# Kernel tuning notes

Measured on AMD Instinct MI355X. Metric: run time of the kernel, lower is better.

Reference implementation:

```python
import jax, jax.numpy as jnp
import numpy as np

N_NODES = 100000
N_EDGES = 1200000
C = 64            # hidden_channels == in_channels
HEADS = 4
HEAD_D = C // HEADS
EDGE_D = 16
N_LAYERS = 3
NUM_GRAPHS = 128


def setup_inputs() -> dict:
    key = jax.random.key(0)
    ks = jax.random.split(key, 24)
    x = jax.random.normal(ks[0], (N_NODES, C), dtype=jnp.float32)
    edge_index = jax.random.randint(ks[1], (2, N_EDGES), 0, N_NODES, dtype=jnp.int64)
    edge_attr = jax.random.normal(ks[2], (N_EDGES, EDGE_D), dtype=jnp.float32)
    batch = jnp.sort(jax.random.randint(ks[3], (N_NODES,), 0, NUM_GRAPHS, dtype=jnp.int64))
    s = 1.0 / np.sqrt(C)
    se = 1.0 / np.sqrt(EDGE_D)
    inp = {
        "x": x, "edge_index": edge_index, "edge_attr": edge_attr, "batch": batch,
        "Wq": jax.random.normal(ks[4], (N_LAYERS, C, C), jnp.float32) * s,
        "bq": jnp.zeros((N_LAYERS, C), jnp.float32),
        "Wk": jax.random.normal(ks[5], (N_LAYERS, C, C), jnp.float32) * s,
        "bk": jnp.zeros((N_LAYERS, C), jnp.float32),
        "Wv": jax.random.normal(ks[6], (N_LAYERS, C, C), jnp.float32) * s,
        "bv": jnp.zeros((N_LAYERS, C), jnp.float32),
        "We": jax.random.normal(ks[7], (N_LAYERS, EDGE_D, C), jnp.float32) * se,
        "be": jnp.zeros((N_LAYERS, C), jnp.float32),
        "Wskip": jax.random.normal(ks[8], (N_LAYERS, C, C), jnp.float32) * s,
        "bskip": jnp.zeros((N_LAYERS, C), jnp.float32),
        "lin1_w": jax.random.normal(ks[9], (C, C), jnp.float32) * s,
        "lin1_b": jnp.zeros((C,), jnp.float32),
        "lin2_w": jax.random.normal(ks[10], (C, 1), jnp.float32) * s,
        "lin2_b": jnp.zeros((1,), jnp.float32),
    }
    return inp


def _transformer_conv(x, src, dst, edge_attr, Wq, bq, Wk, bk, Wv, bv, We, be, Ws, bs):
    """PyG-style TransformerConv: edge-softmax attention with edge features."""
    n = x.shape[0]
    e = src.shape[0]
    q = (x @ Wq + bq)[dst].reshape(e, HEADS, HEAD_D)          # query at target i
    ea = (edge_attr @ We + be).reshape(e, HEADS, HEAD_D)      # shared edge proj
    k = (x @ Wk + bk)[src].reshape(e, HEADS, HEAD_D) + ea
    v = (x @ Wv + bv)[src].reshape(e, HEADS, HEAD_D) + ea
    logit = jnp.einsum('ehd,ehd->eh', q, k) / jnp.sqrt(jnp.float32(HEAD_D))  # [E,H]
    # numerically-stable softmax over edges sharing the same destination node
    m = jax.ops.segment_max(logit, dst, num_segments=n)       # [N,H]
    ex = jnp.exp(logit - m[dst])
    denom = jax.ops.segment_sum(ex, dst, num_segments=n)      # [N,H]
    alpha = ex / jnp.maximum(denom[dst], 1e-16)
    agg = jax.ops.segment_sum(alpha[:, :, None] * v, dst, num_segments=n)   # [N,H,D]
    return agg.reshape(n, HEADS * HEAD_D) + x @ Ws + bs       # root/skip weight


def reference(x, edge_index, edge_attr, batch, Wq, bq, Wk, bk, Wv, bv, We, be,
              Wskip, bskip, lin1_w, lin1_b, lin2_w, lin2_b):
    src, dst = edge_index[0], edge_index[1]
    h = x
    for l in range(N_LAYERS):
        h = _transformer_conv(h, src, dst, edge_attr,
                              Wq[l], bq[l], Wk[l], bk[l], Wv[l], bv[l],
                              We[l], be[l], Wskip[l], bskip[l])
        if l < N_LAYERS - 1:
            h = jax.nn.relu(h)
    # global mean pool over graphs
    sums = jax.ops.segment_sum(h, batch, num_segments=NUM_GRAPHS)            # [G,C]
    cnt = jax.ops.segment_sum(jnp.ones((h.shape[0], 1), h.dtype), batch,
                              num_segments=NUM_GRAPHS)
    pooled = sums / jnp.maximum(cnt, 1.0)
    out = jax.nn.relu(pooled @ lin1_w + lin1_b)
    return (out @ lin2_w + lin2_b).squeeze(-1)                               # [G]
```

## Files before the change

### kernel.cpp

```cpp
#include <hip/hip_runtime.h>
#include <hip/hip_bf16.h>

#define NODES_C 64
#define HEADS 4
#define HEAD_D 16

__device__ __forceinline__ unsigned short f32_to_bf16(float f) {
    unsigned int x = __float_as_uint(f);
    unsigned int r = x + 0x7fffu + ((x >> 16) & 1u);
    return (unsigned short)(r >> 16);
}
#define BF16_DEC(h) __uint_as_float(((unsigned int)(h)) << 16)

__global__ void count_k(const int* __restrict__ dst, int E, int* __restrict__ deg) {
    int e = blockIdx.x * blockDim.x + threadIdx.x;
    if (e < E) atomicAdd(&deg[dst[e]], 1);
}

__global__ __launch_bounds__(1024) void scan_chunk(const int* __restrict__ deg,
                                                   int* __restrict__ excl,
                                                   int* __restrict__ chunkSums, int N) {
    __shared__ int buf[1024];
    int i = blockIdx.x * 1024 + threadIdx.x;
    int v = (i < N) ? deg[i] : 0;
    buf[threadIdx.x] = v;
    __syncthreads();
    for (int off = 1; off < 1024; off <<= 1) {
        int t = (threadIdx.x >= off) ? buf[threadIdx.x - off] : 0;
        __syncthreads();
        buf[threadIdx.x] += t;
        __syncthreads();
    }
    if (i < N) excl[i] = buf[threadIdx.x] - v;
    if (threadIdx.x == 1023) chunkSums[blockIdx.x] = buf[1023];
}

__global__ __launch_bounds__(128) void scan_sums(int* __restrict__ chunkSums, int nChunks) {
    __shared__ int buf[128];
    int v = (threadIdx.x < nChunks) ? chunkSums[threadIdx.x] : 0;
    buf[threadIdx.x] = v;
    __syncthreads();
    for (int off = 1; off < 128; off <<= 1) {
        int t = (threadIdx.x >= off) ? buf[threadIdx.x - off] : 0;
        __syncthreads();
        buf[threadIdx.x] += t;
        __syncthreads();
    }
    if (threadIdx.x < nChunks) chunkSums[threadIdx.x] = buf[threadIdx.x] - v;
}

__global__ void scan_add(int* __restrict__ excl, const int* __restrict__ chunkSums,
                         int N, int E) {
    int i = blockIdx.x * blockDim.x + threadIdx.x;
    if (i < N) excl[i] += chunkSums[i >> 10];
    if (i == 0) excl[N] = E;
}

__global__ void fill_k(const int* __restrict__ dst, int E,
                       const int* __restrict__ row_start, int* __restrict__ cursor,
                       int* __restrict__ csr) {
    int e = blockIdx.x * blockDim.x + threadIdx.x;
    if (e < E) {
        int d = dst[e];
        int pos = atomicAdd(&cursor[d], 1);
        csr[row_start[d] + pos] = e;
    }
}

__global__ void sort_rows_k(const int* __restrict__ row_start, int* __restrict__ csr,
                            int N) {
    int i = blockIdx.x * blockDim.x + threadIdx.x;
    if (i >= N) return;
    int beg = row_start[i], end = row_start[i + 1];
    for (int p = beg + 1; p < end; ++p) {
        int key = csr[p];
        int j = p - 1;
        while (j >= beg && csr[j] > key) { csr[j + 1] = csr[j]; --j; }
        csr[j + 1] = key;
    }
}

__global__ void gather_edges(const int* __restrict__ csr, const int* __restrict__ srcA,
                             const float4* __restrict__ ea4,
                             int* __restrict__ csr_src,
                             unsigned short* __restrict__ csr_eah, int E) {
    int t = blockIdx.x * blockDim.x + threadIdx.x;
    int p = t >> 2, q = t & 3;
    if (p < E) {
        int e = csr[p];
        if (q == 0) csr_src[p] = srcA[e];
        float4 v = ea4[(size_t)e * 4 + q];
        ushort4 h;
        h.x = f32_to_bf16(v.x);  h.y = f32_to_bf16(v.y);
        h.z = f32_to_bf16(v.z);  h.w = f32_to_bf16(v.w);
        *(ushort4*)(csr_eah + (size_t)p * 16 + q * 4) = h;
    }
}

#define GB 16
__global__ __launch_bounds__(128) void gemm_qkvs(
    const float* __restrict__ Hin,
    const float* __restrict__ Wq, const float* __restrict__ bq,
    const float* __restrict__ Wk, const float* __restrict__ bk,
    const float* __restrict__ Wv, const float* __restrict__ bv,
    const float* __restrict__ Ws, const float* __restrict__ bs,
    float* __restrict__ Q, unsigned short* __restrict__ KVh,
    float* __restrict__ Ssk, int N)
{
    int g = threadIdx.x >> 6;
    int c = threadIdx.x & 63;
    const float* W1 = (g == 0) ? Wq : Wv;
    const float* b1 = (g == 0) ? bq : bv;
    const float* W2 = (g == 0) ? Wk : Ws;
    const float* b2 = (g == 0) ? bk : bs;

    float w1[64], w2[64];
#pragma unroll
    for (int t = 0; t < 64; ++t) {
        w1[t] = W1[t * 64 + c];
        w2[t] = W2[t * 64 + c];
    }
    float bias1 = b1[c], bias2 = b2[c];

    __shared__ __align__(16) float hrow[GB][64];

    for (int base = blockIdx.x * GB; base < N; base += gridDim.x * GB) {
        int nn = min(GB, N - base);
        __syncthreads();
        for (int idx = threadIdx.x; idx < nn * 64; idx += 128)
            hrow[idx >> 6][idx & 63] = Hin[base * 64 + idx];
        __syncthreads();
        for (int r = 0; r < nn; ++r) {
            const float4* h4 = (const float4*)hrow[r];
            float acc1 = bias1, acc2 = bias2;
#pragma unroll
            for (int t4 = 0; t4 < 16; ++t4) {
                float4 hv = h4[t4];
                acc1 += hv.x * w1[4 * t4 + 0];
                acc1 += hv.y * w1[4 * t4 + 1];
                acc1 += hv.z * w1[4 * t4 + 2];
                acc1 += hv.w * w1[4 * t4 + 3];
                acc2 += hv.x * w2[4 * t4 + 0];
                acc2 += hv.y * w2[4 * t4 + 1];
                acc2 += hv.z * w2[4 * t4 + 2];
                acc2 += hv.w * w2[4 * t4 + 3];
            }
            size_t row = (size_t)(base + r);
            if (g == 0) {
                Q[row * 64 + c] = acc1;
                KVh[row * 128 + 2 * c] = f32_to_bf16(acc2);
            } else {
                KVh[row * 128 + 2 * c + 1] = f32_to_bf16(acc1);
                Ssk[row * 64 + c] = acc2;
            }
        }
    }
}

#define KV_DECODE(u, kf, vf)                                \
    kf = __uint_as_float((u) << 16);                        \
    vf = __uint_as_float((u) & 0xffff0000u);

__global__ __launch_bounds__(256) void attn_pre(
    const float* __restrict__ Q, const unsigned int* __restrict__ KVu,
    const float* __restrict__ Ssk,
    const int* __restrict__ row_start, const int* __restrict__ csr_src,
    const unsigned short* __restrict__ csr_eah,
    const float* __restrict__ We, const float* __restrict__ be,
    float* __restrict__ Hout, int N, int doRelu)
{
    __shared__ float weS[16 * 68];
    for (int idx = threadIdx.x; idx < 1024; idx += 256)
        weS[(idx >> 6) * 68 + (idx & 63)] = We[idx];
    __syncthreads();

    int lane = threadIdx.x & 63;
    int tl = lane & 15;
    int hb = lane & 48;
    float wcol[16];
#pragma unroll
    for (int t = 0; t < 16; ++t) wcol[t] = weS[t * 68 + lane];
    float beL = be[lane];

    int gwave  = (blockIdx.x * blockDim.x + threadIdx.x) >> 6;
    int nwaves = (gridDim.x * blockDim.x) >> 6;

    const float4* wr4 = (const float4*)(weS + tl * 68 + hb);
    float4 wa = wr4[0], wb = wr4[1], wc4 = wr4[2], wd = wr4[3];

    for (int i = gwave; i < N; i += nwaves) {
        float q = Q[(size_t)i * 64 + lane];

        const float4* qh4 = (const float4*)(Q + (size_t)i * 64 + hb);
        float4 qa = qh4[0], qb4 = qh4[1], qc4 = qh4[2], qd = qh4[3];
        float G = qa.x * wa.x + qa.y * wa.y + qa.z * wa.z + qa.w * wa.w
                + qb4.x * wb.x + qb4.y * wb.y + qb4.z * wb.z + qb4.w * wb.w
                + qc4.x * wc4.x + qc4.y * wc4.y + qc4.z * wc4.z + qc4.w * wc4.w
                + qd.x * wd.x + qd.y * wd.y + qd.z * wd.z + qd.w * wd.w;
        float rb = q * beL;
#pragma unroll
        for (int off = 8; off >= 1; off >>= 1) rb += __shfl_xor(rb, off, 16);
        float qbase = rb * 0.25f;

        int beg = row_start[i], end = row_start[i + 1];
        float m = -INFINITY, s = 0.f, acc = 0.f, z = 0.f;

        int p = beg;
        if (p + 7 < end) {
            int j0 = csr_src[p],     j1 = csr_src[p + 1];
            int j2 = csr_src[p + 2], j3 = csr_src[p + 3];
            int j4 = csr_src[p + 4], j5 = csr_src[p + 5];
            int j6 = csr_src[p + 6], j7 = csr_src[p + 7];
            const unsigned short* eh = csr_eah + (size_t)p * 16 + tl;
            float a0 = BF16_DEC(eh[0]),  a1 = BF16_DEC(eh[16]);
            float a2 = BF16_DEC(eh[32]), a3 = BF16_DEC(eh[48]);
            float a4 = BF16_DEC(eh[64]), a5 = BF16_DEC(eh[80]);
            float a6 = BF16_DEC(eh[96]), a7 = BF16_DEC(eh[112]);

            do {
                unsigned int u0 = KVu[(size_t)j0 * 64 + lane];
                unsigned int u1 = KVu[(size_t)j1 * 64 + lane];
                unsigned int u2 = KVu[(size_t)j2 * 64 + lane];
                unsigned int u3 = KVu[(size_t)j3 * 64 + lane];
                unsigned int u4 = KVu[(size_t)j4 * 64 + lane];
                unsigned int u5 = KVu[(size_t)j5 * 64 + lane];
                unsigned int u6 = KVu[(size_t)j6 * 64 + lane];
                unsigned int u7 = KVu[(size_t)j7 * 64 + lane];

                int pn = p + 8;
                bool more = (pn + 7 < end);
                int jn0 = j0, jn1 = j1, jn2 = j2, jn3 = j3;
                int jn4 = j4, jn5 = j5, jn6 = j6, jn7 = j7;
                float an0 = a0, an1 = a1, an2 = a2, an3 = a3;
                float an4 = a4, an5 = a5, an6 = a6, an7 = a7;
                if (more) {
                    jn0 = csr_src[pn];     jn1 = csr_src[pn + 1];
                    jn2 = csr_src[pn + 2]; jn3 = csr_src[pn + 3];
                    jn4 = csr_src[pn + 4]; jn5 = csr_src[pn + 5];
                    jn6 = csr_src[pn + 6]; jn7 = csr_src[pn + 7];
                    const unsigned short* ehn = csr_eah + (size_t)pn * 16 + tl;
                    an0 = BF16_DEC(ehn[0]);  an1 = BF16_DEC(ehn[16]);
                    an2 = BF16_DEC(ehn[32]); an3 = BF16_DEC(ehn[48]);
                    an4 = BF16_DEC(ehn[64]); an5 = BF16_DEC(ehn[80]);
                    an6 = BF16_DEC(ehn[96]); an7 = BF16_DEC(ehn[112]);
                }

                float k0, v0, k1, v1, k2, v2, k3, v3, k4, v4, k5, v5, k6, v6, k7, v7;
                KV_DECODE(u0, k0, v0)  KV_DECODE(u1, k1, v1)
                KV_DECODE(u2, k2, v2)  KV_DECODE(u3, k3, v3)
                KV_DECODE(u4, k4, v4)  KV_DECODE(u5, k5, v5)
                KV_DECODE(u6, k6, v6)  KV_DECODE(u7, k7, v7)

                float l0 = q * k0 + a0 * G;
                float l1 = q * k1 + a1 * G;
                float l2 = q * k2 + a2 * G;
                float l3 = q * k3 + a3 * G;
                float l4 = q * k4 + a4 * G;
                float l5 = q * k5 + a5 * G;
                float l6 = q * k6 + a6 * G;
                float l7 = q * k7 + a7 * G;
#pragma unroll
                for (int off = 8; off >= 1; off >>= 1) {
                    l0 += __shfl_xor(l0, off, 16);
                    l1 += __shfl_xor(l1, off, 16);
                    l2 += __shfl_xor(l2, off, 16);
                    l3 += __shfl_xor(l3, off, 16);
                    l4 += __shfl_xor(l4, off, 16);
                    l5 += __shfl_xor(l5, off, 16);
                    l6 += __shfl_xor(l6, off, 16);
                    l7 += __shfl_xor(l7, off, 16);
                }
                l0 = l0 * 0.25f + qbase;  l1 = l1 * 0.25f + qbase;
                l2 = l2 * 0.25f + qbase;  l3 = l3 * 0.25f + qbase;
                l4 = l4 * 0.25f + qbase;  l5 = l5 * 0.25f + qbase;
                l6 = l6 * 0.25f + qbase;  l7 = l7 * 0.25f + qbase;

                float nm = fmaxf(fmaxf(fmaxf(l0, l1), fmaxf(l2, l3)),
                                 fmaxf(fmaxf(l4, l5), fmaxf(l6, l7)));
                nm = fmaxf(nm, m);
                float sc = __expf(m - nm);
                float w0 = __expf(l0 - nm), w1 = __expf(l1 - nm);
                float w2 = __expf(l2 - nm), w3 = __expf(l3 - nm);
                float w4 = __expf(l4 - nm), w5 = __expf(l5 - nm);
                float w6 = __expf(l6 - nm), w7 = __expf(l7 - nm);
                s   = s * sc + ((w0 + w1) + (w2 + w3)) + ((w4 + w5) + (w6 + w7));
                acc = acc * sc + ((w0 * v0 + w1 * v1) + (w2 * v2 + w3 * v3))
                               + ((w4 * v4 + w5 * v5) + (w6 * v6 + w7 * v7));
                z   = z * sc + ((w0 * a0 + w1 * a1) + (w2 * a2 + w3 * a3))
                             + ((w4 * a4 + w5 * a5) + (w6 * a6 + w7 * a7));
                m = nm;

                j0 = jn0; j1 = jn1; j2 = jn2; j3 = jn3;
                j4 = jn4; j5 = jn5; j6 = jn6; j7 = jn7;
                a0 = an0; a1 = an1; a2 = an2; a3 = an3;
                a4 = an4; a5 = an5; a6 = an6; a7 = an7;
                p = pn;
            } while (p + 7 < end);
        }
        for (; p + 3 < end; p += 4) {
            int j0 = csr_src[p],     j1 = csr_src[p + 1];
            int j2 = csr_src[p + 2], j3 = csr_src[p + 3];
            unsigned int u0 = KVu[(size_t)j0 * 64 + lane];
            unsigned int u1 = KVu[(size_t)j1 * 64 + lane];
            unsigned int u2 = KVu[(size_t)j2 * 64 + lane];
            unsigned int u3 = KVu[(size_t)j3 * 64 + lane];
            const unsigned short* eh = csr_eah + (size_t)p * 16 + tl;
            float a0 = BF16_DEC(eh[0]),  a1 = BF16_DEC(eh[16]);
            float a2 = BF16_DEC(eh[32]), a3 = BF16_DEC(eh[48]);

            float k0, v0, k1, v1, k2, v2, k3, v3;
            KV_DECODE(u0, k0, v0)  KV_DECODE(u1, k1, v1)
            KV_DECODE(u2, k2, v2)  KV_DECODE(u3, k3, v3)

            float l0 = q * k0 + a0 * G;
            float l1 = q * k1 + a1 * G;
            float l2 = q * k2 + a2 * G;
            float l3 = q * k3 + a3 * G;
#pragma unroll
            for (int off = 8; off >= 1; off >>= 1) {
                l0 += __shfl_xor(l0, off, 16);
                l1 += __shfl_xor(l1, off, 16);
                l2 += __shfl_xor(l2, off, 16);
                l3 += __shfl_xor(l3, off, 16);
            }
            l0 = l0 * 0.25f + qbase;  l1 = l1 * 0.25f + qbase;
            l2 = l2 * 0.25f + qbase;  l3 = l3 * 0.25f + qbase;

            float nm = fmaxf(fmaxf(fmaxf(l0, l1), fmaxf(l2, l3)), m);
            float sc = __expf(m - nm);
            float w0 = __expf(l0 - nm), w1 = __expf(l1 - nm);
            float w2 = __expf(l2 - nm), w3 = __expf(l3 - nm);
            s   = s * sc + w0 + w1 + w2 + w3;
            acc = acc * sc + w0 * v0 + w1 * v1 + w2 * v2 + w3 * v3;
            z   = z * sc + w0 * a0 + w1 * a1 + w2 * a2 + w3 * a3;
            m = nm;
        }
        for (; p < end; ++p) {
            int j = csr_src[p];
            unsigned int u = KVu[(size_t)j * 64 + lane];
            float a = BF16_DEC(csr_eah[(size_t)p * 16 + tl]);
            float kf, vf;
            KV_DECODE(u, kf, vf)
            float l = q * kf + a * G;
#pragma unroll
            for (int off = 8; off >= 1; off >>= 1) l += __shfl_xor(l, off, 16);
            l = l * 0.25f + qbase;
            float nm = fmaxf(m, l);
            float sc = __expf(m - nm);
            float w  = __expf(l - nm);
            s   = s * sc + w;
            acc = acc * sc + w * vf;
            z   = z * sc + w * a;
            m = nm;
        }

        float o;
        if (s > 0.f) {
            float t = acc;
#pragma unroll
            for (int u = 0; u < 16; ++u) t += wcol[u] * __shfl(z, u, 16);
            o = t / s + beL + Ssk[(size_t)i * 64 + lane];
        } else {
            o = Ssk[(size_t)i * 64 + lane];
        }
        if (doRelu) o = fmaxf(o, 0.f);
        Hout[(size_t)i * 64 + lane] = o;
    }
}

__global__ __launch_bounds__(256) void attn_k(
    const float* __restrict__ Q, const unsigned int* __restrict__ KVu,
    const float* __restrict__ Ssk,
    const int* __restrict__ row_start, const int* __restrict__ csr,
    const int* __restrict__ srcA, const float* __restrict__ edge_attr,
    const float* __restrict__ We, const float* __restrict__ be,
    float* __restrict__ Hout, int N, int doRelu)
{
    int lane = threadIdx.x & 63;
    float wcol[16];
#pragma unroll
    for (int t = 0; t < 16; ++t) wcol[t] = We[t * 64 + lane];
    float beL = be[lane];

    int gwave  = (blockIdx.x * blockDim.x + threadIdx.x) >> 6;
    int nwaves = (gridDim.x * blockDim.x) >> 6;

    for (int i = gwave; i < N; i += nwaves) {
        float q = Q[(size_t)i * 64 + lane];
        int beg = row_start[i], end = row_start[i + 1];
        float m = -INFINITY, s = 0.f, acc = 0.f;
        for (int p = beg; p < end; ++p) {
            int e = csr[p];
            int j = srcA[e];
            const float4* ap = (const float4*)(edge_attr + (size_t)e * 16);
            float4 a0 = ap[0], a1 = ap[1], a2 = ap[2], a3 = ap[3];
            unsigned int u = KVu[(size_t)j * 64 + lane];
            float kf, vf;
            KV_DECODE(u, kf, vf)
            float ea = beL;
            ea += a0.x * wcol[0]  + a0.y * wcol[1]  + a0.z * wcol[2]  + a0.w * wcol[3];
            ea += a1.x * wcol[4]  + a1.y * wcol[5]  + a1.z * wcol[6]  + a1.w * wcol[7];
            ea += a2.x * wcol[8]  + a2.y * wcol[9]  + a2.z * wcol[10] + a2.w * wcol[11];
            ea += a3.x * wcol[12] + a3.y * wcol[13] + a3.z * wcol[14] + a3.w * wcol[15];
            float kv = kf + ea, vv = vf + ea;
            float part = q * kv;
#pragma unroll
            for (int off = 8; off >= 1; off >>= 1) part += __shfl_xor(part, off, 16);
            float logit = part * 0.25f;
            float nm = fmaxf(m, logit);
            float sc = __expf(m - nm);
            float w  = __expf(logit - nm);
            s = s * sc + w;  acc = acc * sc + w * vv;  m = nm;
        }
        float agg = (s > 0.f) ? acc / s : 0.f;
        float o = agg + Ssk[(size_t)i * 64 + lane];
        if (doRelu) o = fmaxf(o, 0.f);
        Hout[(size_t)i * 64 + lane] = o;
    }
}

__device__ __forceinline__ int lbound(const int* __restrict__ a, int n, int key) {
    int lo = 0, hi = n;
    while (lo < hi) { int mid = (lo + hi) >> 1; if (a[mid] < key) lo = mid + 1; else hi = mid; }
    return lo;
}

__global__ __launch_bounds__(256) void pool_mean_k(
    const float* __restrict__ H, const int* __restrict__ batch,
    float* __restrict__ pooled, int N)
{
    int g = blockIdx.x;
    int lo = lbound(batch, N, g);
    int hi = lbound(batch, N, g + 1);
    int lane = threadIdx.x & 63;
    int w = threadIdx.x >> 6;

    float acc = 0.f;
    for (int i = lo + w; i < hi; i += 4)
        acc += H[(size_t)i * 64 + lane];

    __shared__ float part[4][64];
    part[w][lane] = acc;
    __syncthreads();
    if (w == 0) {
        float s = ((part[0][lane] + part[1][lane]) + part[2][lane]) + part[3][lane];
        float cnt = (float)(hi - lo);
        pooled[g * 64 + lane] = s / fmaxf(cnt, 1.0f);
    }
}

__global__ __launch_bounds__(64) void mlp_k(
    const float* __restrict__ pooled,
    const float* __restrict__ lin1_w, const float* __restrict__ lin1_b,
    const float* __restrict__ lin2_w, const float* __restrict__ lin2_b,
    float* __restrict__ out)
{
    int g = blockIdx.x;
    int c = threadIdx.x;
    float acc = lin1_b[c];
#pragma unroll
    for (int t = 0; t < 64; ++t) acc += pooled[g * 64 + t] * lin1_w[t * 64 + c];
    float r = fmaxf(acc, 0.f) * lin2_w[c];
#pragma unroll
    for (int off = 32; off >= 1; off >>= 1) r += __shfl_xor(r, off, 64);
    if (c == 0) out[g] = r + lin2_b[0];
}

extern "C" void kernel_launch(void* const* d_in, const int* in_sizes, int n_in,
                              void* d_out, int out_size, void* d_ws, size_t ws_size,
                              hipStream_t stream) {
    const float* x        = (const float*)d_in[0];
    const int*   eidx     = (const int*)  d_in[1];
    const float* eattr    = (const float*)d_in[2];
    const int*   batch    = (const int*)  d_in[3];
    const float* Wq       = (const float*)d_in[4];
    const float* bq       = (const float*)d_in[5];
    const float* Wk       = (const float*)d_in[6];
    const float* bk       = (const float*)d_in[7];
    const float* Wv       = (const float*)d_in[8];
    const float* bv       = (const float*)d_in[9];
    const float* We       = (const float*)d_in[10];
    const float* be       = (const float*)d_in[11];
    const float* Wskip    = (const float*)d_in[12];
    const float* bskip    = (const float*)d_in[13];
    const float* lin1_w   = (const float*)d_in[14];
    const float* lin1_b   = (const float*)d_in[15];
    const float* lin2_w   = (const float*)d_in[16];
    const float* lin2_b   = (const float*)d_in[17];

    int N = in_sizes[0] / 64;
    int E = in_sizes[1] / 2;
    const int* src = eidx;
    const int* dst = eidx + E;

    char* w = (char*)d_ws;
    auto alloc = [&](size_t bytes) {
        char* p = w;
        w += (bytes + 255) & ~(size_t)255;
        return p;
    };
    float* Q   = (float*)alloc((size_t)N * 64 * 4);
    unsigned short* KVh = (unsigned short*)alloc((size_t)N * 128 * 2);
    float* S   = (float*)alloc((size_t)N * 64 * 4);
    float* H   = (float*)alloc((size_t)N * 64 * 4);
    int* deg       = (int*)alloc((size_t)N * 4);
    int* cursor    = (int*)alloc((size_t)N * 4);
    int* row_start = (int*)alloc((size_t)(N + 1) * 4);
    int* csr       = (int*)alloc((size_t)E * 4);
    int* chunkSums = (int*)alloc(128 * 4);
    float* pooled  = (float*)alloc(128 * 64 * 4);
    int* csr_src              = (int*)alloc((size_t)E * 4);
    unsigned short* csr_eah   = (unsigned short*)alloc((size_t)E * 16 * 2);
    bool pre = ((size_t)(w - (char*)d_ws) <= ws_size);

    hipMemsetAsync(deg, 0, (size_t)((char*)cursor - (char*)deg) + (size_t)N * 4, stream);

    count_k<<<(E + 255) / 256, 256, 0, stream>>>(dst, E, deg);
    int nChunks = (N + 1023) / 1024;
    scan_chunk<<<nChunks, 1024, 0, stream>>>(deg, row_start, chunkSums, N);
    scan_sums<<<1, 128, 0, stream>>>(chunkSums, nChunks);
    scan_add<<<(N + 255) / 256, 256, 0, stream>>>(row_start, chunkSums, N, E);
    fill_k<<<(E + 255) / 256, 256, 0, stream>>>(dst, E, row_start, cursor, csr);
    sort_rows_k<<<(N + 255) / 256, 256, 0, stream>>>(row_start, csr, N);

    if (pre) {
        gather_edges<<<((size_t)E * 4 + 255) / 256, 256, 0, stream>>>(
            csr, src, (const float4*)eattr, csr_src, csr_eah, E);
    }

    const float* Hin = x;
    for (int l = 0; l < 3; ++l) {
        gemm_qkvs<<<2048, 128, 0, stream>>>(Hin,
            Wq + l * 4096, bq + l * 64, Wk + l * 4096, bk + l * 64,
            Wv + l * 4096, bv + l * 64, Wskip + l * 4096, bskip + l * 64,
            Q, KVh, S, N);
        if (pre) {
            attn_pre<<<4096, 256, 0, stream>>>(Q, (const unsigned int*)KVh, S,
                row_start, csr_src, csr_eah,
                We + l * 1024, be + l * 64, H, N, (l < 2) ? 1 : 0);
        } else {
            attn_k<<<4096, 256, 0, stream>>>(Q, (const unsigned int*)KVh, S,
                row_start, csr, src, eattr,
                We + l * 1024, be + l * 64, H, N, (l < 2) ? 1 : 0);
        }
        Hin = H;
    }

    pool_mean_k<<<128, 256, 0, stream>>>(Hin, batch, pooled, N);
    mlp_k<<<128, 64, 0, stream>>>(pooled, lin1_w, lin1_b, lin2_w, lin2_b,
                                  (float*)d_out);
}
```

Before: 964.7 us.

## Split attention wave into two half-waves processing alternate edges with 2 channels per lane

Restructures the attn_pre kernel so each lane owns two adjacent channels and the two 32-lane halves of a wave each process a different edge. Per-edge gathers become 8-byte vector loads, the logit reductions shrink from 16-lane to 8-lane shuffles, and the two half-wave online-softmax states are merged at the end with a cross-half shuffle. The aim is to double edge-level parallelism per wave and reduce shuffle and load-instruction counts. In exchange it adds more register pressure (duplicated weights and accumulators) and a final merge step, and drops the explicit software prefetch of the next edge batch.

```diff
diff --git a/kernel.cpp b/kernel.cpp
--- a/kernel.cpp
+++ b/kernel.cpp
@@ -11,6 +11,9 @@
     return (unsigned short)(r >> 16);
 }
 #define BF16_DEC(h) __uint_as_float(((unsigned int)(h)) << 16)
+#define PAIR_DECODE(u, lo, hi)                              \
+    lo = __uint_as_float((u) << 16);                        \
+    hi = __uint_as_float((u) & 0xffff0000u);
 
 __global__ void count_k(const int* __restrict__ dst, int E, int* __restrict__ deg) {
     int e = blockIdx.x * blockDim.x + threadIdx.x;
@@ -157,10 +160,6 @@
     }
 }
 
-#define KV_DECODE(u, kf, vf)                                \
-    kf = __uint_as_float((u) << 16);                        \
-    vf = __uint_as_float((u) & 0xffff0000u);
-
 __global__ __launch_bounds__(256) void attn_pre(
     const float* __restrict__ Q, const unsigned int* __restrict__ KVu,
     const float* __restrict__ Ssk,
@@ -175,198 +174,188 @@
     __syncthreads();
 
     int lane = threadIdx.x & 63;
-    int tl = lane & 15;
-    int hb = lane & 48;
-    float wcol[16];
-#pragma unroll
-    for (int t = 0; t < 16; ++t) wcol[t] = weS[t * 68 + lane];
-    float beL = be[lane];
+    int half = lane >> 5;
+    int l5   = lane & 31;
+    int c0   = 2 * l5;
+    int h    = l5 >> 3;
+    int t0   = 2 * (l5 & 7);
+
+    float wA0[8], wA1[8], wB0[8], wB1[8];
+#pragma unroll
+    for (int u = 0; u < 8; ++u) {
+        wA0[u] = weS[(2 * u) * 68 + c0];
+        wA1[u] = weS[(2 * u + 1) * 68 + c0];
+        wB0[u] = weS[(2 * u) * 68 + c0 + 1];
+        wB1[u] = weS[(2 * u + 1) * 68 + c0 + 1];
+    }
+    float be0 = be[c0], be1 = be[c0 + 1];
 
     int gwave  = (blockIdx.x * blockDim.x + threadIdx.x) >> 6;
     int nwaves = (gridDim.x * blockDim.x) >> 6;
 
-    const float4* wr4 = (const float4*)(weS + tl * 68 + hb);
-    float4 wa = wr4[0], wb = wr4[1], wc4 = wr4[2], wd = wr4[3];
+    const float4* w0r = (const float4*)(weS + t0 * 68 + 16 * h);
+    const float4* w1r = (const float4*)(weS + (t0 + 1) * 68 + 16 * h);
+    float4 wr00 = w0r[0], wr01 = w0r[1], wr02 = w0r[2], wr03 = w0r[3];
+    float4 wr10 = w1r[0], wr11 = w1r[1], wr12 = w1r[2], wr13 = w1r[3];
 
     for (int i = gwave; i < N; i += nwaves) {
-        float q = Q[(size_t)i * 64 + lane];
-
-        const float4* qh4 = (const float4*)(Q + (size_t)i * 64 + hb);
-        float4 qa = qh4[0], qb4 = qh4[1], qc4 = qh4[2], qd = qh4[3];
-        float G = qa.x * wa.x + qa.y * wa.y + qa.z * wa.z + qa.w * wa.w
-                + qb4.x * wb.x + qb4.y * wb.y + qb4.z * wb.z + qb4.w * wb.w
-                + qc4.x * wc4.x + qc4.y * wc4.y + qc4.z * wc4.z + qc4.w * wc4.w
-                + qd.x * wd.x + qd.y * wd.y + qd.z * wd.z + qd.w * wd.w;
-        float rb = q * beL;
-#pragma unroll
-        for (int off = 8; off >= 1; off >>= 1) rb += __shfl_xor(rb, off, 16);
+        float2 qp = *(const float2*)(Q + (size_t)i * 64 + c0);
+        float q0 = qp.x, q1 = qp.y;
+
+        const float4* qh4 = (const float4*)(Q + (size_t)i * 64 + 16 * h);
+        float4 qv0 = qh4[0], qv1 = qh4[1], qv2 = qh4[2], qv3 = qh4[3];
+        float G0 = qv0.x * wr00.x + qv0.y * wr00.y + qv0.z * wr00.z + qv0.w * wr00.w
+                 + qv1.x * wr01.x + qv1.y * wr01.y + qv1.z * wr01.z + qv1.w * wr01.w
+                 + qv2.x * wr02.x + qv2.y * wr02.y + qv2.z * wr02.z + qv2.w * wr02.w
+                 + qv3.x * wr03.x + qv3.y * wr03.y + qv3.z * wr03.z + qv3.w * wr03.w;
+        float G1 = qv0.x * wr10.x + qv0.y * wr10.y + qv0.z * wr10.z + qv0.w * wr10.w
+                 + qv1.x * wr11.x + qv1.y * wr11.y + qv1.z * wr11.z + qv1.w * wr11.w
+                 + qv2.x * wr12.x + qv2.y * wr12.y + qv2.z * wr12.z + qv2.w * wr12.w
+                 + qv3.x * wr13.x + qv3.y * wr13.y + qv3.z * wr13.z + qv3.w * wr13.w;
+
+        float rb = q0 * be0 + q1 * be1;
+        rb += __shfl_xor(rb, 4, 8);
+        rb += __shfl_xor(rb, 2, 8);
+        rb += __shfl_xor(rb, 1, 8);
         float qbase = rb * 0.25f;
 
         int beg = row_start[i], end = row_start[i + 1];
-        float m = -INFINITY, s = 0.f, acc = 0.f, z = 0.f;
+        float m = -INFINITY, s = 0.f, acc0 = 0.f, acc1 = 0.f, z0 = 0.f, z1 = 0.f;
 
         int p = beg;
-        if (p + 7 < end) {
-            int j0 = csr_src[p],     j1 = csr_src[p + 1];
-            int j2 = csr_src[p + 2], j3 = csr_src[p + 3];
-            int j4 = csr_src[p + 4], j5 = csr_src[p + 5];
-            int j6 = csr_src[p + 6], j7 = csr_src[p + 7];
-            const unsigned short* eh = csr_eah + (size_t)p * 16 + tl;
-            float a0 = BF16_DEC(eh[0]),  a1 = BF16_DEC(eh[16]);
-            float a2 = BF16_DEC(eh[32]), a3 = BF16_DEC(eh[48]);
-            float a4 = BF16_DEC(eh[64]), a5 = BF16_DEC(eh[80]);
-            float a6 = BF16_DEC(eh[96]), a7 = BF16_DEC(eh[112]);
-
-            do {
-                unsigned int u0 = KVu[(size_t)j0 * 64 + lane];
-                unsigned int u1 = KVu[(size_t)j1 * 64 + lane];
-                unsigned int u2 = KVu[(size_t)j2 * 64 + lane];
-                unsigned int u3 = KVu[(size_t)j3 * 64 + lane];
-                unsigned int u4 = KVu[(size_t)j4 * 64 + lane];
-                unsigned int u5 = KVu[(size_t)j5 * 64 + lane];
-                unsigned int u6 = KVu[(size_t)j6 * 64 + lane];
-                unsigned int u7 = KVu[(size_t)j7 * 64 + lane];
-
-                int pn = p + 8;
-                bool more = (pn + 7 < end);
-                int jn0 = j0, jn1 = j1, jn2 = j2, jn3 = j3;
-                int jn4 = j4, jn5 = j5, jn6 = j6, jn7 = j7;
-                float an0 = a0, an1 = a1, an2 = a2, an3 = a3;
-                float an4 = a4, an5 = a5, an6 = a6, an7 = a7;
-                if (more) {
-                    jn0 = csr_src[pn];     jn1 = csr_src[pn + 1];
-                    jn2 = csr_src[pn + 2]; jn3 = csr_src[pn + 3];
-                    jn4 = csr_src[pn + 4]; jn5 = csr_src[pn + 5];
-                    jn6 = csr_src[pn + 6]; jn7 = csr_src[pn + 7];
-                    const unsigned short* ehn = csr_eah + (size_t)pn * 16 + tl;
-                    an0 = BF16_DEC(ehn[0]);  an1 = BF16_DEC(ehn[16]);
-                    an2 = BF16_DEC(ehn[32]); an3 = BF16_DEC(ehn[48]);
-                    an4 = BF16_DEC(ehn[64]); an5 = BF16_DEC(ehn[80]);
-                    an6 = BF16_DEC(ehn[96]); an7 = BF16_DEC(ehn[112]);
-                }
-
-                float k0, v0, k1, v1, k2, v2, k3, v3, k4, v4, k5, v5, k6, v6, k7, v7;
-                KV_DECODE(u0, k0, v0)  KV_DECODE(u1, k1, v1)
-                KV_DECODE(u2, k2, v2)  KV_DECODE(u3, k3, v3)
-                KV_DECODE(u4, k4, v4)  KV_DECODE(u5, k5, v5)
-                KV_DECODE(u6, k6, v6)  KV_DECODE(u7, k7, v7)
-
-                float l0 = q * k0 + a0 * G;
-                float l1 = q * k1 + a1 * G;
-                float l2 = q * k2 + a2 * G;
-                float l3 = q * k3 + a3 * G;
-                float l4 = q * k4 + a4 * G;
-                float l5 = q * k5 + a5 * G;
-                float l6 = q * k6 + a6 * G;
-                float l7 = q * k7 + a7 * G;
-#pragma unroll
-                for (int off = 8; off >= 1; off >>= 1) {
-                    l0 += __shfl_xor(l0, off, 16);
-                    l1 += __shfl_xor(l1, off, 16);
-                    l2 += __shfl_xor(l2, off, 16);
-                    l3 += __shfl_xor(l3, off, 16);
-                    l4 += __shfl_xor(l4, off, 16);
-                    l5 += __shfl_xor(l5, off, 16);
-                    l6 += __shfl_xor(l6, off, 16);
-                    l7 += __shfl_xor(l7, off, 16);
-                }
-                l0 = l0 * 0.25f + qbase;  l1 = l1 * 0.25f + qbase;
-                l2 = l2 * 0.25f + qbase;  l3 = l3 * 0.25f + qbase;
-                l4 = l4 * 0.25f + qbase;  l5 = l5 * 0.25f + qbase;
-                l6 = l6 * 0.25f + qbase;  l7 = l7 * 0.25f + qbase;
-
-                float nm = fmaxf(fmaxf(fmaxf(l0, l1), fmaxf(l2, l3)),
-                                 fmaxf(fmaxf(l4, l5), fmaxf(l6, l7)));
-                nm = fmaxf(nm, m);
-                float sc = __expf(m - nm);
-                float w0 = __expf(l0 - nm), w1 = __expf(l1 - nm);
-                float w2 = __expf(l2 - nm), w3 = __expf(l3 - nm);
-                float w4 = __expf(l4 - nm), w5 = __expf(l5 - nm);
-                float w6 = __expf(l6 - nm), w7 = __expf(l7 - nm);
-                s   = s * sc + ((w0 + w1) + (w2 + w3)) + ((w4 + w5) + (w6 + w7));
-                acc = acc * sc + ((w0 * v0 + w1 * v1) + (w2 * v2 + w3 * v3))
-                               + ((w4 * v4 + w5 * v5) + (w6 * v6 + w7 * v7));
-                z   = z * sc + ((w0 * a0 + w1 * a1) + (w2 * a2 + w3 * a3))
-                             + ((w4 * a4 + w5 * a5) + (w6 * a6 + w7 * a7));
-                m = nm;
-
-                j0 = jn0; j1 = jn1; j2 = jn2; j3 = jn3;
-                j4 = jn4; j5 = jn5; j6 = jn6; j7 = jn7;
-                a0 = an0; a1 = an1; a2 = an2; a3 = an3;
-                a4 = an4; a5 = an5; a6 = an6; a7 = an7;
-                p = pn;
-            } while (p + 7 < end);
-        }
-        for (; p + 3 < end; p += 4) {
-            int j0 = csr_src[p],     j1 = csr_src[p + 1];
-            int j2 = csr_src[p + 2], j3 = csr_src[p + 3];
-            unsigned int u0 = KVu[(size_t)j0 * 64 + lane];
-            unsigned int u1 = KVu[(size_t)j1 * 64 + lane];
-            unsigned int u2 = KVu[(size_t)j2 * 64 + lane];
-            unsigned int u3 = KVu[(size_t)j3 * 64 + lane];
-            const unsigned short* eh = csr_eah + (size_t)p * 16 + tl;
-            float a0 = BF16_DEC(eh[0]),  a1 = BF16_DEC(eh[16]);
-            float a2 = BF16_DEC(eh[32]), a3 = BF16_DEC(eh[48]);
-
-            float k0, v0, k1, v1, k2, v2, k3, v3;
-            KV_DECODE(u0, k0, v0)  KV_DECODE(u1, k1, v1)
-            KV_DECODE(u2, k2, v2)  KV_DECODE(u3, k3, v3)
-
-            float l0 = q * k0 + a0 * G;
-            float l1 = q * k1 + a1 * G;
-            float l2 = q * k2 + a2 * G;
-            float l3 = q * k3 + a3 * G;
-#pragma unroll
-            for (int off = 8; off >= 1; off >>= 1) {
-                l0 += __shfl_xor(l0, off, 16);
-                l1 += __shfl_xor(l1, off, 16);
-                l2 += __shfl_xor(l2, off, 16);
-                l3 += __shfl_xor(l3, off, 16);
+        for (; p + 7 < end; p += 8) {
+            int e0 = p + half, e1 = p + 2 + half, e2 = p + 4 + half, e3 = p + 6 + half;
+            int j0 = csr_src[e0], j1 = csr_src[e1];
+            int j2 = csr_src[e2], j3 = csr_src[e3];
+            uint2 kv0 = *(const uint2*)(KVu + (size_t)j0 * 64 + c0);
+            uint2 kv1 = *(const uint2*)(KVu + (size_t)j1 * 64 + c0);
+            uint2 kv2 = *(const uint2*)(KVu + (size_t)j2 * 64 + c0);
+            uint2 kv3 = *(const uint2*)(KVu + (size_t)j3 * 64 + c0);
+            unsigned int ua0 = *(const unsigned int*)(csr_eah + (size_t)e0 * 16 + t0);
+            unsigned int ua1 = *(const unsigned int*)(csr_eah + (size_t)e1 * 16 + t0);
+            unsigned int ua2 = *(const unsigned int*)(csr_eah + (size_t)e2 * 16 + t0);
+            unsigned int ua3 = *(const unsigned int*)(csr_eah + (size_t)e3 * 16 + t0);
+
+            float k00, v00, k01, v01;  PAIR_DECODE(kv0.x, k00, v00)  PAIR_DECODE(kv0.y, k01, v01)
+            float k10, v10, k11, v11;  PAIR_DECODE(kv1.x, k10, v10)  PAIR_DECODE(kv1.y, k11, v11)
+            float k20, v20, k21, v21;  PAIR_DECODE(kv2.x, k20, v20)  PAIR_DECODE(kv2.y, k21, v21)
+            float k30, v30, k31, v31;  PAIR_DECODE(kv3.x, k30, v30)  PAIR_DECODE(kv3.y, k31, v31)
+            float a00, a01;  PAIR_DECODE(ua0, a00, a01)
+            float a10, a11;  PAIR_DECODE(ua1, a10, a11)
+            float a20, a21;  PAIR_DECODE(ua2, a20, a21)
+            float a30, a31;  PAIR_DECODE(ua3, a30, a31)
+
+            float p0 = q0 * k00 + q1 * k01 + a00 * G0 + a01 * G1;
+            float p1 = q0 * k10 + q1 * k11 + a10 * G0 + a11 * G1;
+            float p2 = q0 * k20 + q1 * k21 + a20 * G0 + a21 * G1;
+            float p3 = q0 * k30 + q1 * k31 + a30 * G0 + a31 * G1;
+#pragma unroll
+            for (int off = 4; off >= 1; off >>= 1) {
+                p0 += __shfl_xor(p0, off, 8);
+                p1 += __shfl_xor(p1, off, 8);
+                p2 += __shfl_xor(p2, off, 8);
+                p3 += __shfl_xor(p3, off, 8);
             }
-            l0 = l0 * 0.25f + qbase;  l1 = l1 * 0.25f + qbase;
-            l2 = l2 * 0.25f + qbase;  l3 = l3 * 0.25f + qbase;
+            float l0 = p0 * 0.25f + qbase;
+            float l1 = p1 * 0.25f + qbase;
+            float l2 = p2 * 0.25f + qbase;
+            float l3 = p3 * 0.25f + qbase;
 
             float nm = fmaxf(fmaxf(fmaxf(l0, l1), fmaxf(l2, l3)), m);
             float sc = __expf(m - nm);
             float w0 = __expf(l0 - nm), w1 = __expf(l1 - nm);
             float w2 = __expf(l2 - nm), w3 = __expf(l3 - nm);
-            s   = s * sc + w0 + w1 + w2 + w3;
-            acc = acc * sc + w0 * v0 + w1 * v1 + w2 * v2 + w3 * v3;
-            z   = z * sc + w0 * a0 + w1 * a1 + w2 * a2 + w3 * a3;
+            s    = s * sc + ((w0 + w1) + (w2 + w3));
+            acc0 = acc0 * sc + ((w0 * v00 + w1 * v10) + (w2 * v20 + w3 * v30));
+            acc1 = acc1 * sc + ((w0 * v01 + w1 * v11) + (w2 * v21 + w3 * v31));
+            z0   = z0 * sc + ((w0 * a00 + w1 * a10) + (w2 * a20 + w3 * a30));
+            z1   = z1 * sc + ((w0 * a01 + w1 * a11) + (w2 * a21 + w3 * a31));
             m = nm;
         }
-        for (; p < end; ++p) {
-            int j = csr_src[p];
-            unsigned int u = KVu[(size_t)j * 64 + lane];
-            float a = BF16_DEC(csr_eah[(size_t)p * 16 + tl]);
-            float kf, vf;
-            KV_DECODE(u, kf, vf)
-            float l = q * kf + a * G;
-#pragma unroll
-            for (int off = 8; off >= 1; off >>= 1) l += __shfl_xor(l, off, 16);
-            l = l * 0.25f + qbase;
+        for (; p + 1 < end; p += 2) {
+            int e = p + half;
+            int j = csr_src[e];
+            uint2 kv = *(const uint2*)(KVu + (size_t)j * 64 + c0);
+            unsigned int ua = *(const unsigned int*)(csr_eah + (size_t)e * 16 + t0);
+            float k0, v0, k1, v1;  PAIR_DECODE(kv.x, k0, v0)  PAIR_DECODE(kv.y, k1, v1)
+            float a0, a1;  PAIR_DECODE(ua, a0, a1)
+            float pt = q0 * k0 + q1 * k1 + a0 * G0 + a1 * G1;
+#pragma unroll
+            for (int off = 4; off >= 1; off >>= 1) pt += __shfl_xor(pt, off, 8);
+            float l = pt * 0.25f + qbase;
             float nm = fmaxf(m, l);
             float sc = __expf(m - nm);
             float w  = __expf(l - nm);
-            s   = s * sc + w;
-            acc = acc * sc + w * vf;
-            z   = z * sc + w * a;
+            s    = s * sc + w;
+            acc0 = acc0 * sc + w * v0;
+            acc1 = acc1 * sc + w * v1;
+            z0   = z0 * sc + w * a0;
+            z1   = z1 * sc + w * a1;
             m = nm;
         }
-
-        float o;
+        if (p < end) {
+            int j = csr_src[p];
+            uint2 kv = *(const uint2*)(KVu + (size_t)j * 64 + c0);
+            unsigned int ua = *(const unsigned int*)(csr_eah + (size_t)p * 16 + t0);
+            float k0, v0, k1, v1;  PAIR_DECODE(kv.x, k0, v0)  PAIR_DECODE(kv.y, k1, v1)
+            float a0, a1;  PAIR_DECODE(ua, a0, a1)
+            float pt = q0 * k0 + q1 * k1 + a0 * G0 + a1 * G1;
+#pragma unroll
+            for (int off = 4; off >= 1; off >>= 1) pt += __shfl_xor(pt, off, 8);
+            float l = pt * 0.25f + qbase;
+            if (half == 0) {
+                float nm = fmaxf(m, l);
+                float sc = __expf(m - nm);
+                float w  = __expf(l - nm);
+                s    = s * sc + w;
+                acc0 = acc0 * sc + w * v0;
+                acc1 = acc1 * sc + w * v1;
+                z0   = z0 * sc + w * a0;
+                z1   = z1 * sc + w * a1;
+                m = nm;
+            }
+        }
+
+        float mo  = __shfl_xor(m, 32);
+        float so  = __shfl_xor(s, 32);
+        float ao0 = __shfl_xor(acc0, 32);
+        float ao1 = __shfl_xor(acc1, 32);
+        float zo0 = __shfl_xor(z0, 32);
+        float zo1 = __shfl_xor(z1, 32);
+        float nmm = fmaxf(m, mo);
+        float cs = __expf(m - nmm), co = __expf(mo - nmm);
+        s    = s * cs + so * co;
+        acc0 = acc0 * cs + ao0 * co;
+        acc1 = acc1 * cs + ao1 * co;
+        z0   = z0 * cs + zo0 * co;
+        z1   = z1 * cs + zo1 * co;
+
+        float2 sk = *(const float2*)(Ssk + (size_t)i * 64 + c0);
+        float o0, o1;
         if (s > 0.f) {
-            float t = acc;
-#pragma unroll
-            for (int u = 0; u < 16; ++u) t += wcol[u] * __shfl(z, u, 16);
-            o = t / s + beL + Ssk[(size_t)i * 64 + lane];
+            float t0v = acc0, t1v = acc1;
+#pragma unroll
+            for (int u = 0; u < 8; ++u) {
+                float zz0 = __shfl(z0, u, 8);
+                float zz1 = __shfl(z1, u, 8);
+                t0v += wA0[u] * zz0 + wA1[u] * zz1;
+                t1v += wB0[u] * zz0 + wB1[u] * zz1;
+            }
+            o0 = t0v / s + be0 + sk.x;
+            o1 = t1v / s + be1 + sk.y;
         } else {
-            o = Ssk[(size_t)i * 64 + lane];
-        }
-        if (doRelu) o = fmaxf(o, 0.f);
-        Hout[(size_t)i * 64 + lane] = o;
-    }
-}
+            o0 = sk.x;
+            o1 = sk.y;
+        }
+        if (doRelu) { o0 = fmaxf(o0, 0.f); o1 = fmaxf(o1, 0.f); }
+        if (half == 0)
+            *(float2*)(Hout + (size_t)i * 64 + c0) = make_float2(o0, o1);
+    }
+}
+
+#define KV_DECODE(u, kf, vf)                                \
+    kf = __uint_as_float((u) << 16);                        \
+    vf = __uint_as_float((u) & 0xffff0000u);
 
 __global__ __launch_bounds__(256) void attn_k(
     const float* __restrict__ Q, const unsigned int* __restrict__ KVu,
```

Result: slower. 1.035 ms (+7.3%).
